# Optimization experiments

Hardware: AMD Instinct MI355X
Metric: run time of the kernel (lower is better)

The kernel has to match this reference:

```python
import jax, jax.numpy as jnp
import numpy as np

RS, RC = 3.0, 6.0
N_AXIS = 8
N_NODES, N_ENV, N_EDGES = 50000, 1000000, 200000
N_ATOM = 4
NEURONS = [32, 64, 64]


def setup_inputs() -> dict:
    key = jax.random.key(0)
    ks = jax.random.split(key, 10)
    env_vectors = jax.random.normal(ks[0], (N_ENV, 3), dtype=jnp.float32) * 2.0
    atom_attr = jax.random.uniform(ks[1], (N_NODES, N_ATOM), dtype=jnp.float32)
    env_index = jax.random.randint(ks[2], (2, N_ENV), 0, N_NODES)
    edge_index = jax.random.randint(ks[3], (2, N_EDGES), 0, N_NODES)
    d_in = 2 * N_ATOM + 1  # snorm + both endpoint one-hot attrs
    W1 = jax.random.normal(ks[4], (d_in, NEURONS[0]), dtype=jnp.float32) / np.sqrt(d_in)
    b1 = jnp.zeros((NEURONS[0],), jnp.float32)
    W2 = jax.random.normal(ks[5], (NEURONS[0], NEURONS[1]), dtype=jnp.float32) / np.sqrt(NEURONS[0])
    b2 = jnp.zeros((NEURONS[1],), jnp.float32)
    W3 = jax.random.normal(ks[6], (NEURONS[1], NEURONS[2]), dtype=jnp.float32) / np.sqrt(NEURONS[1])
    b3 = jnp.zeros((NEURONS[2],), jnp.float32)
    return dict(env_vectors=env_vectors, atom_attr=atom_attr, env_index=env_index,
                edge_index=edge_index, W1=W1, b1=b1, W2=W2, b2=b2, W3=W3, b3=b3)


def _smooth(r):
    # elementwise smooth cutoff: 1/r for r<rs, polynomial taper on [rs,rc), 0 beyond
    x = (r - RC) / (RS - RC)
    mid = (1.0 / r) * (x ** 3 * (10.0 + x * (-15.0 + 6.0 * x)) + 1.0)
    return jnp.where(r < RS, 1.0 / r, jnp.where(r < RC, mid, jnp.zeros_like(r)))


def reference(env_vectors, atom_attr, env_index, edge_index, W1, b1, W2, b2, W3, b3):
    n_env = env_vectors.shape[0]
    n_nodes = atom_attr.shape[0]
    r = jnp.linalg.norm(env_vectors, axis=-1, keepdims=True)          # [E,1]
    snorm = _smooth(r)
    # gather both endpoint attrs: env_index.T.flatten() interleaves (src_i, dst_i)
    env_attr = atom_attr[env_index.T.reshape(-1)].reshape(n_env, -1)  # [E, 2*n_atom]
    # ResNet embedding (residual where dims match)
    h = jnp.tanh(jnp.concatenate([snorm, env_attr], axis=-1) @ W1 + b1)
    h = jnp.tanh(h @ W2 + b2)
    h = jnp.tanh(h @ W3 + b3) + h                                     # [E, D]
    # outer product with direction vectors, scatter-mean over target node
    outer = h[:, :, None] * env_vectors[:, None, :]                   # [E, D, 3]
    idx = env_index[1]
    summ = jax.ops.segment_sum(outer, idx, num_segments=n_nodes)      # [N, D, 3]
    cnt = jax.ops.segment_sum(jnp.ones((n_env,), h.dtype), idx, num_segments=n_nodes)
    aggr = summ / jnp.clip(cnt, 1.0)[:, None, None]
    # per-node self outer-product bmm, slice first n_axis columns, flatten
    desc = jnp.einsum('nda,nea->nde', aggr, aggr)[:, :, :N_AXIS]      # [N, D, n_axis]
    node_desc = desc.reshape(n_nodes, -1)                             # [N, D*n_axis]
    edge_desc = node_desc[edge_index[0]] + node_desc[edge_index[1]]   # [Ne, D*n_axis]
    return node_desc, edge_desc
```

## Files before the change

### kernel.cpp

```cpp
#include <hip/hip_runtime.h>
#include <hip/hip_bf16.h>

#define N_NODES 50000
#define N_ENV   1000000
#define N_EDGES 200000

__device__ __forceinline__ float fast_tanh(float x){
  float xc = fminf(fmaxf(x, -10.f), 10.f);
  float t  = __expf(2.f * xc);
  return __fdividef(t - 1.f, t + 1.f);
}

__global__ void k_zero_i(int* __restrict__ p, int n){
  int i = blockIdx.x * blockDim.x + threadIdx.x;
  int stride = gridDim.x * blockDim.x;
  for (; i < n; i += stride) p[i] = 0;
}

__global__ __launch_bounds__(256) void k_hist(
    const int* __restrict__ env_index, int* __restrict__ counts)
{
  int e = blockIdx.x * 256 + threadIdx.x;
  if (e >= N_ENV) return;
  atomicAdd(counts + env_index[N_ENV + e], 1);
}

__global__ __launch_bounds__(1024) void k_scan(
    const int* __restrict__ counts, int* __restrict__ offsets,
    int* __restrict__ cursor)
{
  __shared__ int wsum[16];
  __shared__ int s_carry, s_tot;
  int tid = threadIdx.x, lane = tid & 63, w = tid >> 6;
  if (tid == 0) s_carry = 0;
  __syncthreads();
  for (int base = 0; base < N_NODES; base += 8192){
    int i0 = base + tid * 8;
    int c[8];
    #pragma unroll
    for (int j = 0; j < 8; j++){ int i = i0 + j; c[j] = (i < N_NODES) ? counts[i] : 0; }
    int local = 0;
    #pragma unroll
    for (int j = 0; j < 8; j++) local += c[j];
    int incl = local;
    #pragma unroll
    for (int off = 1; off < 64; off <<= 1){
      int t = __shfl_up(incl, off);
      if (lane >= off) incl += t;
    }
    if (lane == 63) wsum[w] = incl;
    __syncthreads();
    if (w == 0 && lane < 16){
      int v = wsum[lane];
      int winc = v;
      #pragma unroll
      for (int off = 1; off < 16; off <<= 1){
        int t = __shfl_up(winc, off);
        if (lane >= off) winc += t;
      }
      wsum[lane] = winc - v;
      if (lane == 15) s_tot = winc;
    }
    __syncthreads();
    int run = s_carry + wsum[w] + incl - local;
    #pragma unroll
    for (int j = 0; j < 8; j++){
      int i = i0 + j;
      if (i < N_NODES){ offsets[i] = run; cursor[i] = run; }
      run += c[j];
    }
    __syncthreads();
    if (tid == 0) s_carry += s_tot;
    __syncthreads();
  }
}

__global__ __launch_bounds__(256) void k_scatter(
    const int* __restrict__ env_index, int* __restrict__ cursor,
    int* __restrict__ order)
{
  int e = blockIdx.x * 256 + threadIdx.x;
  if (e >= N_ENV) return;
  int dst = env_index[N_ENV + e];
  int pos = atomicAdd(cursor + dst, 1);
  order[pos] = e;
}

__global__ __launch_bounds__(256) void k_mlp(
    const float* __restrict__ env_vec, const float* __restrict__ atom_attr,
    const int*  __restrict__ env_index,
    const float* __restrict__ W1, const float* __restrict__ B1,
    const float* __restrict__ W2, const float* __restrict__ B2,
    const float* __restrict__ W3, const float* __restrict__ B3,
    float* __restrict__ h_out)
{
  __shared__ float sW1[32*9];
  __shared__ float sW2[64*32];
  __shared__ float sW3[64*64];
  __shared__ float sB1[32], sB2[64], sB3[64];
  __shared__ float stage[512*17];
  for (int k = threadIdx.x; k < 32*9;  k += 256){ int j = k/9,  i = k%9;  sW1[k] = W1[i*32+j]; }
  for (int k = threadIdx.x; k < 64*32; k += 256){ int j = k>>5, i = k&31; sW2[k] = W2[i*64+j]; }
  for (int k = threadIdx.x; k < 64*64; k += 256){ int j = k>>6, i = k&63; sW3[k] = W3[i*64+j]; }
  if (threadIdx.x < 32) sB1[threadIdx.x] = B1[threadIdx.x];
  if (threadIdx.x < 64) sB2[threadIdx.x] = B2[threadIdx.x];
  if (threadIdx.x < 64) sB3[threadIdx.x] = B3[threadIdx.x];
  __syncthreads();

  const int tid  = threadIdx.x;
  const int base = blockIdx.x * 512;
  int eA = base + tid;
  int eB = eA + 256;
  int elA = min(eA, N_ENV - 1);
  int elB = min(eB, N_ENV - 1);

  float xA[9], xB[9];
  {
    float v0 = env_vec[3*elA+0], v1 = env_vec[3*elA+1], v2 = env_vec[3*elA+2];
    float r = sqrtf(v0*v0 + v1*v1 + v2*v2);
    float invr = 1.f / r;
    float xx = (r - 6.f) * (-1.f/3.f);
    float mid = invr * (xx*xx*xx*(10.f + xx*(-15.f + 6.f*xx)) + 1.f);
    xA[0] = (r < 3.f) ? invr : ((r < 6.f) ? mid : 0.f);
    int src = env_index[elA], dst = env_index[N_ENV + elA];
    float4 sa = *reinterpret_cast<const float4*>(atom_attr + src*4);
    float4 da = *reinterpret_cast<const float4*>(atom_attr + dst*4);
    xA[1]=sa.x; xA[2]=sa.y; xA[3]=sa.z; xA[4]=sa.w;
    xA[5]=da.x; xA[6]=da.y; xA[7]=da.z; xA[8]=da.w;
  }
  {
    float v0 = env_vec[3*elB+0], v1 = env_vec[3*elB+1], v2 = env_vec[3*elB+2];
    float r = sqrtf(v0*v0 + v1*v1 + v2*v2);
    float invr = 1.f / r;
    float xx = (r - 6.f) * (-1.f/3.f);
    float mid = invr * (xx*xx*xx*(10.f + xx*(-15.f + 6.f*xx)) + 1.f);
    xB[0] = (r < 3.f) ? invr : ((r < 6.f) ? mid : 0.f);
    int src = env_index[elB], dst = env_index[N_ENV + elB];
    float4 sa = *reinterpret_cast<const float4*>(atom_attr + src*4);
    float4 da = *reinterpret_cast<const float4*>(atom_attr + dst*4);
    xB[1]=sa.x; xB[2]=sa.y; xB[3]=sa.z; xB[4]=sa.w;
    xB[5]=da.x; xB[6]=da.y; xB[7]=da.z; xB[8]=da.w;
  }

  float h1A[32], h1B[32];
  #pragma unroll
  for (int j = 0; j < 32; j++){
    float accA = sB1[j], accB = sB1[j];
    #pragma unroll
    for (int i = 0; i < 9; i++){ float w = sW1[j*9 + i]; accA += xA[i]*w; accB += xB[i]*w; }
    h1A[j] = fast_tanh(accA);
    h1B[j] = fast_tanh(accB);
  }

  float h2A[64], h2B[64];
  #pragma unroll
  for (int j = 0; j < 64; j++){
    float accA = sB2[j], accB = sB2[j];
    #pragma unroll
    for (int i = 0; i < 32; i++){ float w = sW2[j*32 + i]; accA += h1A[i]*w; accB += h1B[i]*w; }
    h2A[j] = fast_tanh(accA);
    h2B[j] = fast_tanh(accB);
  }

  #pragma unroll
  for (int c = 0; c < 4; c++){
    #pragma unroll
    for (int dd = 0; dd < 16; dd++){
      int d = c*16 + dd;
      float accA = sB3[d], accB = sB3[d];
      #pragma unroll
      for (int i = 0; i < 64; i++){ float w = sW3[d*64 + i]; accA += h2A[i]*w; accB += h2B[i]*w; }
      stage[tid*17 + dd]       = fast_tanh(accA) + h2A[d];
      stage[(tid+256)*17 + dd] = fast_tanh(accB) + h2B[d];
    }
    __syncthreads();
    int rb = tid >> 2;
    int j  = tid & 3;
    #pragma unroll
    for (int p = 0; p < 8; p++){
      int rr = p*64 + rb;
      float w0 = stage[rr*17 + j*4 + 0];
      float w1 = stage[rr*17 + j*4 + 1];
      float w2 = stage[rr*17 + j*4 + 2];
      float w3 = stage[rr*17 + j*4 + 3];
      int erow = base + rr;
      if (erow < N_ENV)
        *reinterpret_cast<float4*>(h_out + (size_t)erow*64 + c*16 + j*4) =
            make_float4(w0, w1, w2, w3);
    }
    __syncthreads();
  }
}

__global__ __launch_bounds__(256) void k_aggr_node(
    const float* __restrict__ h, const float* __restrict__ env_vec,
    const int* __restrict__ offsets, const int* __restrict__ counts,
    const int* __restrict__ order, float* __restrict__ node_out)
{
  int wid  = (blockIdx.x * 256 + threadIdx.x) >> 6;
  int lane = threadIdx.x & 63;
  if (wid >= N_NODES) return;
  int off = offsets[wid];
  int c   = counts[wid];

  float a0 = 0.f, a1 = 0.f, a2 = 0.f;
  if (c > 0){
    int e = __builtin_amdgcn_readfirstlane(order[off]);
    float hv = h[(size_t)e * 64 + lane];
    for (int k = 0; k < c; k++){
      int en = (k + 1 < c) ? __builtin_amdgcn_readfirstlane(order[off + k + 1]) : e;
      float hv_n = h[(size_t)en * 64 + lane];
      float v0 = env_vec[3*e+0];
      float v1 = env_vec[3*e+1];
      float v2 = env_vec[3*e+2];
      a0 += hv * v0;
      a1 += hv * v1;
      a2 += hv * v2;
      e = en; hv = hv_n;
    }
  }
  float inv = 1.f / fmaxf((float)c, 1.f);
  a0 *= inv; a1 *= inv; a2 *= inv;

  float o[8];
  #pragma unroll
  for (int e2 = 0; e2 < 8; e2++){
    float b0 = __shfl(a0, e2);
    float b1 = __shfl(a1, e2);
    float b2 = __shfl(a2, e2);
    o[e2] = a0*b0 + a1*b1 + a2*b2;
  }
  float* dst = node_out + (size_t)wid * 512 + lane * 8;
  *reinterpret_cast<float4*>(dst)     = make_float4(o[0], o[1], o[2], o[3]);
  *reinterpret_cast<float4*>(dst + 4) = make_float4(o[4], o[5], o[6], o[7]);
}

__global__ __launch_bounds__(256) void k_edge(
    const float* __restrict__ node_out, const int* __restrict__ edge_index,
    float* __restrict__ edge_out)
{
  int t = threadIdx.x;
  int e = blockIdx.x * 2 + (t >> 7);
  int l = t & 127;
  int s  = edge_index[e];
  int dn = edge_index[N_EDGES + e];
  const float4* rs = reinterpret_cast<const float4*>(node_out + (size_t)s  * 512);
  const float4* rd = reinterpret_cast<const float4*>(node_out + (size_t)dn * 512);
  float4 a = rs[l];
  float4 b = rd[l];
  float4 o = make_float4(a.x + b.x, a.y + b.y, a.z + b.z, a.w + b.w);
  reinterpret_cast<float4*>(edge_out + (size_t)e * 512)[l] = o;
}

extern "C" void kernel_launch(void* const* d_in, const int* in_sizes, int n_in,
                              void* d_out, int out_size, void* d_ws, size_t ws_size,
                              hipStream_t stream) {
  const float* env_vec    = (const float*)d_in[0];
  const float* atom_attr  = (const float*)d_in[1];
  const int*   env_index  = (const int*)  d_in[2];
  const int*   edge_index = (const int*)  d_in[3];
  const float* W1 = (const float*)d_in[4];
  const float* B1 = (const float*)d_in[5];
  const float* W2 = (const float*)d_in[6];
  const float* B2 = (const float*)d_in[7];
  const float* W3 = (const float*)d_in[8];
  const float* B3 = (const float*)d_in[9];

  float* out      = (float*)d_out;
  float* node_out = out;
  float* edge_out = out + (size_t)N_NODES * 512;

  float* scratch = edge_out;
  float* h       = scratch;
  int*   counts  = (int*)(scratch + 64000000);
  int*   offsets = (int*)(scratch + 64100000);
  int*   cursor  = (int*)(scratch + 64200000);
  int*   order   = (int*)(scratch + 64300000);

  k_zero_i<<<196, 256, 0, stream>>>(counts, N_NODES);

  k_hist<<<(N_ENV + 255) / 256, 256, 0, stream>>>(env_index, counts);

  k_scan<<<1, 1024, 0, stream>>>(counts, offsets, cursor);

  k_scatter<<<(N_ENV + 255) / 256, 256, 0, stream>>>(env_index, cursor, order);

  k_mlp<<<(N_ENV + 511) / 512, 256, 0, stream>>>(
      env_vec, atom_attr, env_index, W1, B1, W2, B2, W3, B3, h);

  k_aggr_node<<<(N_NODES + 3) / 4, 256, 0, stream>>>(
      h, env_vec, offsets, counts, order, node_out);

  k_edge<<<N_EDGES / 2, 256, 0, stream>>>(node_out, edge_index, edge_out);
}
```

Baseline: 1.265 ms.

## Pack env vectors into sorted order array and use nontemporal edge stores

The scatter kernel now writes each env entry's index together with its direction vector into a 16-byte record in CSR order. The aggregation kernel reads this record sequentially, replacing the random env_vec gather that depended on the order lookup. The edge output, a large write-once stream, is written with nontemporal stores to reduce cache pollution. In exchange, the scatter writes four times more data, and the per-entry record load is now a vector load rather than a readfirstlane scalar load.

Result: slower. 1.322 ms (+4.5%).

```diff
diff --git a/kernel.cpp b/kernel.cpp
--- a/kernel.cpp
+++ b/kernel.cpp
@@ -4,6 +4,8 @@
 #define N_NODES 50000
 #define N_ENV   1000000
 #define N_EDGES 200000
+
+typedef float f4nt __attribute__((ext_vector_type(4)));
 
 __device__ __forceinline__ float fast_tanh(float x){
   float xc = fminf(fmaxf(x, -10.f), 10.f);
@@ -76,14 +78,17 @@
 }
 
 __global__ __launch_bounds__(256) void k_scatter(
-    const int* __restrict__ env_index, int* __restrict__ cursor,
-    int* __restrict__ order)
+    const int* __restrict__ env_index, const float* __restrict__ env_vec,
+    int* __restrict__ cursor, int4* __restrict__ order4)
 {
   int e = blockIdx.x * 256 + threadIdx.x;
   if (e >= N_ENV) return;
   int dst = env_index[N_ENV + e];
+  float v0 = env_vec[3*e+0];
+  float v1 = env_vec[3*e+1];
+  float v2 = env_vec[3*e+2];
   int pos = atomicAdd(cursor + dst, 1);
-  order[pos] = e;
+  order4[pos] = make_int4(e, __float_as_int(v0), __float_as_int(v1), __float_as_int(v2));
 }
 
 __global__ __launch_bounds__(256) void k_mlp(
@@ -193,9 +198,9 @@
 }
 
 __global__ __launch_bounds__(256) void k_aggr_node(
-    const float* __restrict__ h, const float* __restrict__ env_vec,
+    const float* __restrict__ h, const int4* __restrict__ order4,
     const int* __restrict__ offsets, const int* __restrict__ counts,
-    const int* __restrict__ order, float* __restrict__ node_out)
+    float* __restrict__ node_out)
 {
   int wid  = (blockIdx.x * 256 + threadIdx.x) >> 6;
   int lane = threadIdx.x & 63;
@@ -205,18 +210,15 @@
 
   float a0 = 0.f, a1 = 0.f, a2 = 0.f;
   if (c > 0){
-    int e = __builtin_amdgcn_readfirstlane(order[off]);
-    float hv = h[(size_t)e * 64 + lane];
+    int4  q  = order4[off];
+    float hv = h[(size_t)q.x * 64 + lane];
     for (int k = 0; k < c; k++){
-      int en = (k + 1 < c) ? __builtin_amdgcn_readfirstlane(order[off + k + 1]) : e;
-      float hv_n = h[(size_t)en * 64 + lane];
-      float v0 = env_vec[3*e+0];
-      float v1 = env_vec[3*e+1];
-      float v2 = env_vec[3*e+2];
-      a0 += hv * v0;
-      a1 += hv * v1;
-      a2 += hv * v2;
-      e = en; hv = hv_n;
+      int4  qn  = (k + 1 < c) ? order4[off + k + 1] : q;
+      float hvn = h[(size_t)qn.x * 64 + lane];
+      a0 += hv * __int_as_float(q.y);
+      a1 += hv * __int_as_float(q.z);
+      a2 += hv * __int_as_float(q.w);
+      q = qn; hv = hvn;
     }
   }
   float inv = 1.f / fmaxf((float)c, 1.f);
@@ -248,8 +250,8 @@
   const float4* rd = reinterpret_cast<const float4*>(node_out + (size_t)dn * 512);
   float4 a = rs[l];
   float4 b = rd[l];
-  float4 o = make_float4(a.x + b.x, a.y + b.y, a.z + b.z, a.w + b.w);
-  reinterpret_cast<float4*>(edge_out + (size_t)e * 512)[l] = o;
+  f4nt o = { a.x + b.x, a.y + b.y, a.z + b.z, a.w + b.w };
+  __builtin_nontemporal_store(o, reinterpret_cast<f4nt*>(edge_out + (size_t)e * 512) + l);
 }
 
 extern "C" void kernel_launch(void* const* d_in, const int* in_sizes, int n_in,
@@ -275,7 +277,7 @@
   int*   counts  = (int*)(scratch + 64000000);
   int*   offsets = (int*)(scratch + 64100000);
   int*   cursor  = (int*)(scratch + 64200000);
-  int*   order   = (int*)(scratch + 64300000);
+  int4*  order4  = (int4*)(scratch + 64300000);
 
   k_zero_i<<<196, 256, 0, stream>>>(counts, N_NODES);
 
@@ -283,13 +285,13 @@
 
   k_scan<<<1, 1024, 0, stream>>>(counts, offsets, cursor);
 
-  k_scatter<<<(N_ENV + 255) / 256, 256, 0, stream>>>(env_index, cursor, order);
+  k_scatter<<<(N_ENV + 255) / 256, 256, 0, stream>>>(env_index, env_vec, cursor, order4);
 
   k_mlp<<<(N_ENV + 511) / 512, 256, 0, stream>>>(
       env_vec, atom_attr, env_index, W1, B1, W2, B2, W3, B3, h);
 
   k_aggr_node<<<(N_NODES + 3) / 4, 256, 0, stream>>>(
-      h, env_vec, offsets, counts, order, node_out);
+      h, order4, offsets, counts, node_out);
 
   k_edge<<<N_EDGES / 2, 256, 0, stream>>>(node_out, edge_index, edge_out);
 }
```
